# Kernel optimization log

Hardware: AMD Instinct MI355X
Metric: run time of the kernel (lower is better)

Reference implementation:

```python
import jax, jax.numpy as jnp
import numpy as np
import math

H = 12
DH = 64
MAX_POS = 1024

def setup_inputs() -> dict:
    key = jax.random.key(0)
    ks = jax.random.split(key, 8)
    B, L, D = 2, 1024, 768
    s = 0.02
    return {
        "hidden_states": jax.random.normal(ks[0], (B, L, D), jnp.float32),
        "attention_mask": jnp.zeros((B, 1, 1, L), jnp.float32),
        "struct_matrix": jax.random.uniform(ks[1], (5, B, 1, L, L), jnp.float32),
        "Wq": jax.random.normal(ks[2], (D, D), jnp.float32) * s,
        "bq": jnp.zeros((D,), jnp.float32),
        "Wk": jax.random.normal(ks[3], (D, D), jnp.float32) * s,
        "bk": jnp.zeros((D,), jnp.float32),
        "Wv": jax.random.normal(ks[4], (D, D), jnp.float32) * s,
        "bv": jnp.zeros((D,), jnp.float32),
        "dist_emb": jax.random.normal(ks[5], (2 * MAX_POS - 1, DH), jnp.float32) * s,
        "ssan_w": jax.random.normal(ks[6], (5, H, DH, DH), jnp.float32) * s,
        "abs_bias": jnp.zeros((5, H), jnp.float32),
    }

def reference(hidden_states, attention_mask, struct_matrix, Wq, bq, Wk, bk, Wv, bv, dist_emb, ssan_w, abs_bias):
    B, L, D = hidden_states.shape

    def heads(x):  # [B,L,D] -> [B,H,L,dh]
        return x.reshape(B, L, H, DH).transpose(0, 2, 1, 3)

    q = heads(hidden_states @ Wq + bq)
    k = heads(hidden_states @ Wk + bk)
    v = heads(hidden_states @ Wv + bv)

    scores = jnp.einsum('bhqd,bhkd->bhqk', q, k)

    # relative_key_query positional scores
    pos_ids = jnp.arange(L)
    distance = pos_ids[:, None] - pos_ids[None, :]          # [L,L]
    pos = dist_emb[distance + MAX_POS - 1]                  # [L,L,dh]
    scores = scores + jnp.einsum('bhld,lrd->bhlr', q, pos)
    scores = scores + jnp.einsum('bhrd,lrd->bhlr', k, pos)

    scores = scores / math.sqrt(DH)
    scores = scores + attention_mask

    # 5 SSAN bilinear bias terms, masked by structural matrices
    for i in range(5):
        bias = jnp.einsum('bhqd,hde,bhke->bhqk', q, ssan_w[i], k)
        scores = scores + (bias + abs_bias[i][None, :, None, None]) * struct_matrix[i]

    probs = jax.nn.softmax(scores, axis=-1)
    ctx = jnp.einsum('bhqk,bhkd->bqhd', probs, v).reshape(B, L, D)
    return ctx
```

## Files before the change

### kernel.cpp

```cpp
#include <hip/hip_runtime.h>
#include <math.h>

#define NB 2
#define NL 1024
#define ND 768
#define NH 12
#define DH 64

typedef _Float16 f16;
typedef _Float16 f16x4 __attribute__((ext_vector_type(4)));
typedef _Float16 f16x8 __attribute__((ext_vector_type(8)));
typedef float f32x4 __attribute__((ext_vector_type(4)));

#define MFMA16(a, b, c) __builtin_amdgcn_mfma_f32_16x16x32_f16((a), (b), (c), 0, 0, 0)

__device__ __forceinline__ void soft_barrier() {
    asm volatile("s_waitcnt lgkmcnt(0)\n\ts_barrier" ::: "memory");
}

__global__ __launch_bounds__(256) void prep_kernel(
    const float* __restrict__ hs,
    const float* __restrict__ Wq, const float* __restrict__ Wk,
    const float* __restrict__ Wv, const float* __restrict__ sw,
    const float* __restrict__ de,
    f16* __restrict__ hsf, f16* __restrict__ wt, f16* __restrict__ swt,
    f16* __restrict__ de16)
{
    __shared__ float sT[64 * 66];
    const int t = threadIdx.x;
    const int tile = blockIdx.x;

    if (tile < 768) {
        const int base = tile * 2048 + t * 8;
        float4 a = *(const float4*)&hs[base];
        float4 b = *(const float4*)&hs[base + 4];
        f16x8 hv;
        hv[0] = (f16)a.x; hv[1] = (f16)a.y; hv[2] = (f16)a.z; hv[3] = (f16)a.w;
        hv[4] = (f16)b.x; hv[5] = (f16)b.y; hv[6] = (f16)b.z; hv[7] = (f16)b.w;
        *(f16x8*)&hsf[base] = hv;
        return;
    }
    if (tile >= 1260) {
        const int base = (tile - 1260) * 2048 + t * 8;
        if (base < 2047 * 64) {
            float4 a = *(const float4*)&de[base];
            float4 b = *(const float4*)&de[base + 4];
            f16x8 hv;
            hv[0] = (f16)a.x; hv[1] = (f16)a.y; hv[2] = (f16)a.z; hv[3] = (f16)a.w;
            hv[4] = (f16)b.x; hv[5] = (f16)b.y; hv[6] = (f16)b.z; hv[7] = (f16)b.w;
            *(f16x8*)&de16[base] = hv;
        }
        return;
    }

    const float* S; f16* D; int sRS, dRS;
    const int ti = tile - 768;
    if (ti < 432) {
        const int mat = ti / 144, r2 = ti % 144, ht = r2 / 12, kt = r2 % 12;
        const float* W = (mat == 0) ? Wq : (mat == 1) ? Wk : Wv;
        S = W + (size_t)(kt * 64) * ND + ht * 64;
        D = wt + (size_t)((mat * NH + ht) * 64) * ND + kt * 64;
        sRS = ND; dRS = ND;
    } else {
        const int i = ti - 432;
        S = sw + (size_t)i * 4096;
        D = swt + (size_t)i * 4096;
        sRS = 64; dRS = 64;
    }

    {
        const int kk = t >> 2, nb = (t & 3) * 16;
        float v[16];
        #pragma unroll
        for (int j = 0; j < 4; ++j)
            *(float4*)&v[4 * j] = *(const float4*)&S[(size_t)kk * sRS + nb + 4 * j];
        #pragma unroll
        for (int jj = 0; jj < 16; ++jj)
            sT[(nb + jj) * 66 + kk] = v[jj];
    }
    soft_barrier();
    {
        const int n = t >> 2, kb = (t & 3) * 16;
        f16 tmp[16];
        #pragma unroll
        for (int j = 0; j < 8; ++j) {
            float2 x = *(float2*)&sT[n * 66 + kb + 2 * j];
            tmp[2 * j]     = (f16)x.x;
            tmp[2 * j + 1] = (f16)x.y;
        }
        *(f16x8*)&D[(size_t)n * dRS + kb]     = *(f16x8*)&tmp[0];
        *(f16x8*)&D[(size_t)n * dRS + kb + 8] = *(f16x8*)&tmp[8];
    }
}

__global__ __launch_bounds__(256, 4) void qkv_kernel(
    const f16* __restrict__ hsf, const f16* __restrict__ wt,
    const float* __restrict__ bq, const float* __restrict__ bk,
    const float* __restrict__ bv,
    f16* __restrict__ qf, f16* __restrict__ kf, f16* __restrict__ vt)
{
    __shared__ f16 sA[64 * 72], sB[64 * 72];
    __shared__ float sT[64 * 66];

    const int m0  = blockIdx.x * 64;
    const int y   = blockIdx.y;
    const int mat = y / NH, h = y % NH;
    const int t = threadIdx.x, lane = t & 63, w = t >> 6;
    const int quad = lane >> 4, l15 = lane & 15;
    const int wm = w >> 1, wn = w & 1;

    const float* bias = (mat == 0) ? bq : (mat == 1) ? bk : bv;

    f32x4 acc[2][2];
    #pragma unroll
    for (int r = 0; r < 2; ++r)
        #pragma unroll
        for (int c = 0; c < 2; ++c) acc[r][c] = (f32x4){0.f, 0.f, 0.f, 0.f};

    const int srow = t >> 2, scol = (t & 3) * 16;
    const f16* Ag = hsf + (size_t)(m0 + srow) * ND + scol;
    const f16* Bg = wt + ((size_t)y * 64 + srow) * ND + scol;

    for (int k0 = 0; k0 < ND; k0 += 64) {
        soft_barrier();
        *(f16x8*)&sA[srow * 72 + scol]     = *(const f16x8*)&Ag[k0];
        *(f16x8*)&sA[srow * 72 + scol + 8] = *(const f16x8*)&Ag[k0 + 8];
        *(f16x8*)&sB[srow * 72 + scol]     = *(const f16x8*)&Bg[k0];
        *(f16x8*)&sB[srow * 72 + scol + 8] = *(const f16x8*)&Bg[k0 + 8];
        soft_barrier();
        #pragma unroll
        for (int kk = 0; kk < 64; kk += 32) {
            const int ko = kk + quad * 8;
            f16x8 a0 = *(f16x8*)&sA[(32 * wm + l15) * 72 + ko];
            f16x8 a1 = *(f16x8*)&sA[(32 * wm + 16 + l15) * 72 + ko];
            f16x8 b0 = *(f16x8*)&sB[(32 * wn + l15) * 72 + ko];
            f16x8 b1 = *(f16x8*)&sB[(32 * wn + 16 + l15) * 72 + ko];
            acc[0][0] = MFMA16(a0, b0, acc[0][0]);
            acc[0][1] = MFMA16(a0, b1, acc[0][1]);
            acc[1][0] = MFMA16(a1, b0, acc[1][0]);
            acc[1][1] = MFMA16(a1, b1, acc[1][1]);
        }
    }
    soft_barrier();

    const int bb = m0 >> 10;
    const int lbase = m0 & 1023;
    const int bh = bb * NH + h;

    if (mat < 2) {
        #pragma unroll
        for (int r = 0; r < 2; ++r)
            #pragma unroll
            for (int c = 0; c < 2; ++c) {
                const int col = 32 * wn + 16 * c + l15;
                const float bz = bias[h * 64 + col];
                #pragma unroll
                for (int rr = 0; rr < 4; ++rr)
                    sT[(32 * wm + 16 * r + 4 * quad + rr) * 66 + col] = acc[r][c][rr] + bz;
            }
        soft_barrier();
        const int orow = t >> 2, ocb = (t & 3) * 16;
        f16 tmp[16];
        #pragma unroll
        for (int j = 0; j < 8; ++j) {
            float2 x = *(float2*)&sT[orow * 66 + ocb + 2 * j];
            tmp[2 * j] = (f16)x.x; tmp[2 * j + 1] = (f16)x.y;
        }
        f16* dst = ((mat == 0) ? qf : kf) + ((size_t)bh * NL + lbase + orow) * DH + ocb;
        *(f16x8*)dst       = *(f16x8*)&tmp[0];
        *(f16x8*)(dst + 8) = *(f16x8*)&tmp[8];
    } else {
        #pragma unroll
        for (int r = 0; r < 2; ++r)
            #pragma unroll
            for (int c = 0; c < 2; ++c) {
                const int col = 32 * wn + 16 * c + l15;
                const float bz = bias[h * 64 + col];
                #pragma unroll
                for (int rr = 0; rr < 4; ++rr)
                    sT[col * 66 + 32 * wm + 16 * r + 4 * quad + rr] = acc[r][c][rr] + bz;
            }
        soft_barrier();
        const int d = t >> 2, lcb = (t & 3) * 16;
        f16 tmp[16];
        #pragma unroll
        for (int j = 0; j < 8; ++j) {
            float2 x = *(float2*)&sT[d * 66 + lcb + 2 * j];
            tmp[2 * j] = (f16)x.x; tmp[2 * j + 1] = (f16)x.y;
        }
        f16* dst = vt + ((size_t)bh * DH + d) * NL + lbase + lcb;
        *(f16x8*)dst       = *(f16x8*)&tmp[0];
        *(f16x8*)(dst + 8) = *(f16x8*)&tmp[8];
    }
}

__global__ __launch_bounds__(256, 4) void qw_kernel(
    const f16* __restrict__ qf, const f16* __restrict__ swt,
    f16* __restrict__ qwf)
{
    __shared__ f16 sA[64 * 72], sB[64 * 72];
    __shared__ float sT[64 * 66];

    const int l0 = blockIdx.x * 64;
    const int z  = blockIdx.y;
    const int p  = z / 24, bh = z % 24, h = bh % NH;
    const int t = threadIdx.x, lane = t & 63, w = t >> 6;
    const int quad = lane >> 4, l15 = lane & 15;
    const int wm = w >> 1, wn = w & 1;

    const int srow = t >> 2, scol = (t & 3) * 16;
    {
        const f16* As = qf + ((size_t)bh * NL + l0 + srow) * DH + scol;
        const f16* Bs = swt + ((size_t)(p * NH + h) * 64 + srow) * 64 + scol;
        *(f16x8*)&sA[srow * 72 + scol]     = *(const f16x8*)As;
        *(f16x8*)&sA[srow * 72 + scol + 8] = *(const f16x8*)(As + 8);
        *(f16x8*)&sB[srow * 72 + scol]     = *(const f16x8*)Bs;
        *(f16x8*)&sB[srow * 72 + scol + 8] = *(const f16x8*)(Bs + 8);
    }
    soft_barrier();

    f32x4 acc[2][2];
    #pragma unroll
    for (int r = 0; r < 2; ++r)
        #pragma unroll
        for (int c = 0; c < 2; ++c) acc[r][c] = (f32x4){0.f, 0.f, 0.f, 0.f};

    #pragma unroll
    for (int kk = 0; kk < 64; kk += 32) {
        const int ko = kk + quad * 8;
        f16x8 a0 = *(f16x8*)&sA[(32 * wm + l15) * 72 + ko];
        f16x8 a1 = *(f16x8*)&sA[(32 * wm + 16 + l15) * 72 + ko];
        f16x8 b0 = *(f16x8*)&sB[(32 * wn + l15) * 72 + ko];
        f16x8 b1 = *(f16x8*)&sB[(32 * wn + 16 + l15) * 72 + ko];
        acc[0][0] = MFMA16(a0, b0, acc[0][0]);
        acc[0][1] = MFMA16(a0, b1, acc[0][1]);
        acc[1][0] = MFMA16(a1, b0, acc[1][0]);
        acc[1][1] = MFMA16(a1, b1, acc[1][1]);
    }
    soft_barrier();

    #pragma unroll
    for (int r = 0; r < 2; ++r)
        #pragma unroll
        for (int c = 0; c < 2; ++c) {
            const int col = 32 * wn + 16 * c + l15;
            #pragma unroll
            for (int rr = 0; rr < 4; ++rr)
                sT[(32 * wm + 16 * r + 4 * quad + rr) * 66 + col] = acc[r][c][rr];
        }
    soft_barrier();

    const int orow = t >> 2, ocb = (t & 3) * 16;
    f16 tmp[16];
    #pragma unroll
    for (int j = 0; j < 8; ++j) {
        float2 x = *(float2*)&sT[orow * 66 + ocb + 2 * j];
        tmp[2 * j] = (f16)x.x; tmp[2 * j + 1] = (f16)x.y;
    }
    f16* dst = qwf + ((size_t)(p * 24 + bh) * NL + l0 + orow) * DH + ocb;
    *(f16x8*)dst       = *(f16x8*)&tmp[0];
    *(f16x8*)(dst + 8) = *(f16x8*)&tmp[8];
}

__global__ __launch_bounds__(256, 2) void pos_kernel(
    const f16* __restrict__ qf, const f16* __restrict__ kf,
    const f16* __restrict__ de16, f16* __restrict__ posb)
{
    __shared__ f16 sQ[64 * 72], sK2[64 * 72];
    __shared__ f16 sE[128 * 72];
    __shared__ f16 sQE[64 * 140], sKE[64 * 140];

    const int l0 = blockIdx.x * 64;
    const int r0 = blockIdx.y * 64;
    const int bh = blockIdx.z;
    const int t  = threadIdx.x;
    const int lane = t & 63;
    const int w    = t >> 6;
    const int quad = lane >> 4;
    const int l15  = lane & 15;

    {
        const int row = t >> 3, col = (t & 7) * 8;
        const f16* qs = qf + ((size_t)bh * NL + l0) * DH;
        const f16* ks = kf + ((size_t)bh * NL + r0) * DH;
        *(f16x8*)&sQ[row * 72 + col]        = *(const f16x8*)&qs[row * 64 + col];
        *(f16x8*)&sQ[(row + 32) * 72 + col] = *(const f16x8*)&qs[(row + 32) * 64 + col];
        *(f16x8*)&sK2[row * 72 + col]        = *(const f16x8*)&ks[row * 64 + col];
        *(f16x8*)&sK2[(row + 32) * 72 + col] = *(const f16x8*)&ks[(row + 32) * 64 + col];
        const int ebase = l0 - r0 + 960;
        #pragma unroll
        for (int p = 0; p < 4; ++p) {
            const int er = row + 32 * p;
            if (er < 127)
                *(f16x8*)&sE[er * 72 + col] =
                    *(const f16x8*)&de16[(size_t)(ebase + er) * DH + col];
        }
    }
    soft_barrier();

    {
        const int arow = (16 * w + l15) * 72 + quad * 8;
        f16x8 aq0 = *(f16x8*)&sQ[arow];
        f16x8 aq1 = *(f16x8*)&sQ[arow + 32];
        f16x8 ak0 = *(f16x8*)&sK2[arow];
        f16x8 ak1 = *(f16x8*)&sK2[arow + 32];
        #pragma unroll
        for (int n = 0; n < 8; ++n) {
            const int brow = (16 * n + l15) * 72 + quad * 8;
            f16x8 e0 = *(f16x8*)&sE[brow];
            f16x8 e1 = *(f16x8*)&sE[brow + 32];
            f32x4 cq = {0.f, 0.f, 0.f, 0.f};
            cq = MFMA16(aq0, e0, cq);
            cq = MFMA16(aq1, e1, cq);
            f32x4 ck = {0.f, 0.f, 0.f, 0.f};
            ck = MFMA16(ak0, e0, ck);
            ck = MFMA16(ak1, e1, ck);
            #pragma unroll
            for (int r = 0; r < 4; ++r) {
                sQE[(16 * w + 4 * quad + r) * 140 + 16 * n + l15] = (f16)cq[r];
                sKE[(16 * w + 4 * quad + r) * 140 + 16 * n + l15] = (f16)ck[r];
            }
        }
    }
    soft_barrier();

    {
        const int i  = t >> 2;
        const int j0 = (t & 3) * 16;
        f16 res[16];
        #pragma unroll
        for (int jj = 0; jj < 16; ++jj) {
            const int j = j0 + jj;
            const int tt = i - j + 63;
            float v = (float)sQE[i * 140 + tt] + (float)sKE[j * 140 + tt];
            res[jj] = (f16)v;
        }
        f16* dst = posb + ((size_t)bh * NL + l0 + i) * NL + r0 + j0;
        *(f16x8*)dst       = *(f16x8*)&res[0];
        *(f16x8*)(dst + 8) = *(f16x8*)&res[8];
    }
}

__global__ __launch_bounds__(256, 2) void attn_kernel(
    const f16* __restrict__ qf, const f16* __restrict__ kf,
    const f16* __restrict__ vt, const f16* __restrict__ qwf,
    const float* __restrict__ mask, const float* __restrict__ struct_m,
    const f16* __restrict__ posb, const float* __restrict__ abs_bias,
    float* __restrict__ out)
{
    __shared__ f16 sK[64 * 72];
    __shared__ f16 sVt[2][64 * 72];
    __shared__ float sS[32 * 68];
    __shared__ f16 sP[32 * 72];
    __shared__ float sAlpha[32], sL[32];

    const int l0 = blockIdx.x * 32;
    const int bh = blockIdx.y;
    const int bb = bh / NH, h = bh % NH;
    const int t  = threadIdx.x;
    const int lane  = t & 63;
    const int w     = t >> 6;
    const int quad  = lane >> 4;
    const int l15   = lane & 15;
    const int msub  = w >> 1;
    const int npair = w & 1;

    const size_t NQKV = (size_t)NB * NH * NL * DH;

    f16x8 aQ[2], aW[5][2];
    {
        const size_t qrow = ((size_t)bh * NL + l0 + 16 * msub + l15) * DH;
        #pragma unroll
        for (int K = 0; K < 2; ++K) {
            aQ[K] = *(const f16x8*)&qf[qrow + 32 * K + 8 * quad];
            #pragma unroll
            for (int p = 0; p < 5; ++p)
                aW[p][K] = *(const f16x8*)&qwf[p * NQKV + qrow + 32 * K + 8 * quad];
        }
    }

    float ab[5];
    #pragma unroll
    for (int p = 0; p < 5; ++p) ab[p] = abs_bias[p * NH + h];

    float pf_st[5][2][4], pf_pos[2][4], pf_mask[2];

    auto stage_kv = [&](int r0s, int buf) {
        const int row = t >> 3, col = (t & 7) * 8;
        const f16* ks = kf + ((size_t)bh * NL + r0s) * DH;
        *(f16x8*)&sK[row * 72 + col]        = *(const f16x8*)&ks[row * 64 + col];
        *(f16x8*)&sK[(row + 32) * 72 + col] = *(const f16x8*)&ks[(row + 32) * 64 + col];
        const f16* vs = vt + (size_t)bh * DH * NL + r0s;
        *(f16x8*)&sVt[buf][row * 72 + col] =
            *(const f16x8*)&vs[(size_t)row * NL + col];
        *(f16x8*)&sVt[buf][(row + 32) * 72 + col] =
            *(const f16x8*)&vs[(size_t)(row + 32) * NL + col];
    };

    auto prefetch = [&](int r0s) {
        #pragma unroll
        for (int n = 0; n < 2; ++n) {
            const int j = 32 * npair + 16 * n + l15;
            pf_mask[n] = mask[bb * NL + r0s + j];
            #pragma unroll
            for (int r = 0; r < 4; ++r) {
                const int i = 16 * msub + 4 * quad + r;
                pf_pos[n][r] = (float)posb[((size_t)bh * NL + l0 + i) * NL + r0s + j];
                #pragma unroll
                for (int p = 0; p < 5; ++p)
                    pf_st[p][n][r] =
                        struct_m[((size_t)(p * NB + bb) * NL + l0 + i) * NL + r0s + j];
            }
        }
    };

    stage_kv(0, 0);
    prefetch(0);

    const int sm_i = t >> 3;
    const int sm_jb = t & 7;
    float m_cur = -INFINITY, l_cur = 0.f;
    f32x4 O[2];
    O[0] = (f32x4){0.f, 0.f, 0.f, 0.f};
    O[1] = (f32x4){0.f, 0.f, 0.f, 0.f};

    for (int kt = 0; kt < 16; ++kt) {
        const int cur = kt & 1;
        soft_barrier();

        {
            f32x4 acc[2][6];
            #pragma unroll
            for (int n = 0; n < 2; ++n)
                #pragma unroll
                for (int p = 0; p < 6; ++p)
                    acc[n][p] = (f32x4){0.f, 0.f, 0.f, 0.f};

            #pragma unroll
            for (int K = 0; K < 2; ++K) {
                const int koff = K * 32 + quad * 8;
                f16x8 bk2[2];
                #pragma unroll
                for (int n = 0; n < 2; ++n)
                    bk2[n] = *(f16x8*)&sK[(32 * npair + 16 * n + l15) * 72 + koff];
                #pragma unroll
                for (int n = 0; n < 2; ++n)
                    acc[n][0] = MFMA16(aQ[K], bk2[n], acc[n][0]);
                #pragma unroll
                for (int p = 0; p < 5; ++p)
                    #pragma unroll
                    for (int n = 0; n < 2; ++n)
                        acc[n][1 + p] = MFMA16(aW[p][K], bk2[n], acc[n][1 + p]);
            }

            #pragma unroll
            for (int n = 0; n < 2; ++n) {
                const int j = 32 * npair + 16 * n + l15;
                #pragma unroll
                for (int r = 0; r < 4; ++r) {
                    const int i = 16 * msub + 4 * quad + r;
                    float s = (acc[n][0][r] + pf_pos[n][r]) * 0.125f + pf_mask[n];
                    #pragma unroll
                    for (int p = 0; p < 5; ++p)
                        s += (acc[n][1 + p][r] + ab[p]) * pf_st[p][n][r];
                    sS[i * 68 + j] = s;
                }
            }
        }
        soft_barrier();

        {
            float sv[8];
            float smax = -INFINITY;
            #pragma unroll
            for (int k = 0; k < 8; ++k) {
                sv[k] = sS[sm_i * 68 + sm_jb + 8 * k];
                smax = fmaxf(smax, sv[k]);
            }
            #pragma unroll
            for (int off = 4; off > 0; off >>= 1)
                smax = fmaxf(smax, __shfl_xor(smax, off, 8));
            const float m_new = fmaxf(m_cur, smax);
            const float alpha = __expf(m_cur - m_new);
            float rsum = 0.f;
            #pragma unroll
            for (int k = 0; k < 8; ++k) {
                float p = __expf(sv[k] - m_new);
                sP[sm_i * 72 + sm_jb + 8 * k] = (f16)p;
                rsum += p;
            }
            #pragma unroll
            for (int off = 4; off > 0; off >>= 1)
                rsum += __shfl_xor(rsum, off, 8);
            l_cur = l_cur * alpha + rsum;
            m_cur = m_new;
            if (sm_jb == 0) { sAlpha[sm_i] = alpha; sL[sm_i] = l_cur; }
        }
        soft_barrier();

        {
            if (kt < 15) {
                stage_kv((kt + 1) * 64, cur ^ 1);
                prefetch((kt + 1) * 64);
            }

            float a4[4];
            #pragma unroll
            for (int r = 0; r < 4; ++r) a4[r] = sAlpha[16 * msub + 4 * quad + r];
            #pragma unroll
            for (int n = 0; n < 2; ++n)
                #pragma unroll
                for (int r = 0; r < 4; ++r) O[n][r] *= a4[r];

            const int prow = (16 * msub + l15) * 72;
            #pragma unroll
            for (int K = 0; K < 2; ++K) {
                const int koff = K * 32 + quad * 8;
                f16x8 pfr = *(f16x8*)&sP[prow + koff];
                #pragma unroll
                for (int n = 0; n < 2; ++n) {
                    f16x8 vfr = *(f16x8*)&sVt[cur][(32 * npair + 16 * n + l15) * 72 + koff];
                    O[n] = MFMA16(pfr, vfr, O[n]);
                }
            }
        }
    }

    float linv[4];
    #pragma unroll
    for (int r = 0; r < 4; ++r) linv[r] = 1.0f / sL[16 * msub + 4 * quad + r];
    #pragma unroll
    for (int n = 0; n < 2; ++n) {
        const int dh = 32 * npair + 16 * n + l15;
        #pragma unroll
        for (int r = 0; r < 4; ++r) {
            const int i = 16 * msub + 4 * quad + r;
            out[((size_t)bb * NL + l0 + i) * ND + h * DH + dh] = O[n][r] * linv[r];
        }
    }
}

extern "C" void kernel_launch(void* const* d_in, const int* in_sizes, int n_in,
                              void* d_out, int out_size, void* d_ws, size_t ws_size,
                              hipStream_t stream) {
    const float* hs   = (const float*)d_in[0];
    const float* mask = (const float*)d_in[1];
    const float* stm  = (const float*)d_in[2];
    const float* Wq   = (const float*)d_in[3];
    const float* bq   = (const float*)d_in[4];
    const float* Wk   = (const float*)d_in[5];
    const float* bk   = (const float*)d_in[6];
    const float* Wv   = (const float*)d_in[7];
    const float* bv   = (const float*)d_in[8];
    const float* de   = (const float*)d_in[9];
    const float* sw   = (const float*)d_in[10];
    const float* abb  = (const float*)d_in[11];
    float* outp = (float*)d_out;

    const size_t NQKV = (size_t)NB * NH * NL * DH;
    char* ws = (char*)d_ws;
    f16* qf   = (f16*)ws;                 ws += NQKV * 2;
    f16* kf   = (f16*)ws;                 ws += NQKV * 2;
    f16* vtb  = (f16*)ws;                 ws += NQKV * 2;
    f16* qwf  = (f16*)ws;                 ws += 5 * NQKV * 2;
    f16* posb = (f16*)ws;                 ws += (size_t)24 * 1024 * 1024 * 2;
    f16* de16 = (f16*)ws;
    f16* hsf = posb;
    f16* wt  = hsf + NQKV;
    f16* swt = wt + (size_t)2304 * 768;

    prep_kernel<<<1324, 256, 0, stream>>>(hs, Wq, Wk, Wv, sw, de,
                                          hsf, wt, swt, de16);
    qkv_kernel<<<dim3(32, 36), 256, 0, stream>>>(hsf, wt, bq, bk, bv, qf, kf, vtb);
    qw_kernel<<<dim3(16, 120), 256, 0, stream>>>(qf, swt, qwf);
    pos_kernel<<<dim3(16, 16, 24), 256, 0, stream>>>(qf, kf, de16, posb);
    attn_kernel<<<dim3(32, 24), 256, 0, stream>>>(qf, kf, vtb, qwf,
                                                  mask, stm, posb, abb, outp);
}
```

Baseline: 246.0 us.

## Fuse relative-position score computation into attention kernel, drop posb buffer

Removes the separate pos_kernel, which wrote a 24x1024x1024 fp16 positional-score matrix, and computes the q·E and k·E relative-position products inside the attention kernel for each 32x64 tile. Each tile stages the 95 needed distance-embedding rows into shared memory and runs extra MFMAs, then gathers along the diagonal. This avoids a large global write and read round trip. In exchange it adds MFMA work, an extra barrier per tile, and more shared memory, which could lower occupancy.

New measurement: 243.2 us. No clear change (-1.2%).

```diff
diff --git a/kernel.cpp b/kernel.cpp
--- a/kernel.cpp
+++ b/kernel.cpp
@@ -262,94 +262,18 @@
     *(f16x8*)(dst + 8) = *(f16x8*)&tmp[8];
 }
 
-__global__ __launch_bounds__(256, 2) void pos_kernel(
-    const f16* __restrict__ qf, const f16* __restrict__ kf,
-    const f16* __restrict__ de16, f16* __restrict__ posb)
-{
-    __shared__ f16 sQ[64 * 72], sK2[64 * 72];
-    __shared__ f16 sE[128 * 72];
-    __shared__ f16 sQE[64 * 140], sKE[64 * 140];
-
-    const int l0 = blockIdx.x * 64;
-    const int r0 = blockIdx.y * 64;
-    const int bh = blockIdx.z;
-    const int t  = threadIdx.x;
-    const int lane = t & 63;
-    const int w    = t >> 6;
-    const int quad = lane >> 4;
-    const int l15  = lane & 15;
-
-    {
-        const int row = t >> 3, col = (t & 7) * 8;
-        const f16* qs = qf + ((size_t)bh * NL + l0) * DH;
-        const f16* ks = kf + ((size_t)bh * NL + r0) * DH;
-        *(f16x8*)&sQ[row * 72 + col]        = *(const f16x8*)&qs[row * 64 + col];
-        *(f16x8*)&sQ[(row + 32) * 72 + col] = *(const f16x8*)&qs[(row + 32) * 64 + col];
-        *(f16x8*)&sK2[row * 72 + col]        = *(const f16x8*)&ks[row * 64 + col];
-        *(f16x8*)&sK2[(row + 32) * 72 + col] = *(const f16x8*)&ks[(row + 32) * 64 + col];
-        const int ebase = l0 - r0 + 960;
-        #pragma unroll
-        for (int p = 0; p < 4; ++p) {
-            const int er = row + 32 * p;
-            if (er < 127)
-                *(f16x8*)&sE[er * 72 + col] =
-                    *(const f16x8*)&de16[(size_t)(ebase + er) * DH + col];
-        }
-    }
-    soft_barrier();
-
-    {
-        const int arow = (16 * w + l15) * 72 + quad * 8;
-        f16x8 aq0 = *(f16x8*)&sQ[arow];
-        f16x8 aq1 = *(f16x8*)&sQ[arow + 32];
-        f16x8 ak0 = *(f16x8*)&sK2[arow];
-        f16x8 ak1 = *(f16x8*)&sK2[arow + 32];
-        #pragma unroll
-        for (int n = 0; n < 8; ++n) {
-            const int brow = (16 * n + l15) * 72 + quad * 8;
-            f16x8 e0 = *(f16x8*)&sE[brow];
-            f16x8 e1 = *(f16x8*)&sE[brow + 32];
-            f32x4 cq = {0.f, 0.f, 0.f, 0.f};
-            cq = MFMA16(aq0, e0, cq);
-            cq = MFMA16(aq1, e1, cq);
-            f32x4 ck = {0.f, 0.f, 0.f, 0.f};
-            ck = MFMA16(ak0, e0, ck);
-            ck = MFMA16(ak1, e1, ck);
-            #pragma unroll
-            for (int r = 0; r < 4; ++r) {
-                sQE[(16 * w + 4 * quad + r) * 140 + 16 * n + l15] = (f16)cq[r];
-                sKE[(16 * w + 4 * quad + r) * 140 + 16 * n + l15] = (f16)ck[r];
-            }
-        }
-    }
-    soft_barrier();
-
-    {
-        const int i  = t >> 2;
-        const int j0 = (t & 3) * 16;
-        f16 res[16];
-        #pragma unroll
-        for (int jj = 0; jj < 16; ++jj) {
-            const int j = j0 + jj;
-            const int tt = i - j + 63;
-            float v = (float)sQE[i * 140 + tt] + (float)sKE[j * 140 + tt];
-            res[jj] = (f16)v;
-        }
-        f16* dst = posb + ((size_t)bh * NL + l0 + i) * NL + r0 + j0;
-        *(f16x8*)dst       = *(f16x8*)&res[0];
-        *(f16x8*)(dst + 8) = *(f16x8*)&res[8];
-    }
-}
-
 __global__ __launch_bounds__(256, 2) void attn_kernel(
     const f16* __restrict__ qf, const f16* __restrict__ kf,
     const f16* __restrict__ vt, const f16* __restrict__ qwf,
     const float* __restrict__ mask, const float* __restrict__ struct_m,
-    const f16* __restrict__ posb, const float* __restrict__ abs_bias,
+    const f16* __restrict__ de16, const float* __restrict__ abs_bias,
     float* __restrict__ out)
 {
     __shared__ f16 sK[64 * 72];
     __shared__ f16 sVt[2][64 * 72];
+    __shared__ f16 sE[96 * 72];
+    __shared__ f16 sQEl[96 * 34];
+    __shared__ f16 sKEl[96 * 66];
     __shared__ float sS[32 * 68];
     __shared__ f16 sP[32 * 72];
     __shared__ float sAlpha[32], sL[32];
@@ -383,7 +307,7 @@
     #pragma unroll
     for (int p = 0; p < 5; ++p) ab[p] = abs_bias[p * NH + h];
 
-    float pf_st[5][2][4], pf_pos[2][4], pf_mask[2];
+    float pf_st[5][2][4], pf_mask[2];
 
     auto stage_kv = [&](int r0s, int buf) {
         const int row = t >> 3, col = (t & 7) * 8;
@@ -397,6 +321,18 @@
             *(const f16x8*)&vs[(size_t)(row + 32) * NL + col];
     };
 
+    auto stage_E = [&](int r0s) {
+        const int ebase = l0 - r0s + 960;
+        #pragma unroll
+        for (int p = 0; p < 3; ++p) {
+            const int idx = t + 256 * p;
+            const int er = idx >> 3, col = (idx & 7) * 8;
+            if (er < 95)
+                *(f16x8*)&sE[er * 72 + col] =
+                    *(const f16x8*)&de16[(size_t)(ebase + er) * DH + col];
+        }
+    };
+
     auto prefetch = [&](int r0s) {
         #pragma unroll
         for (int n = 0; n < 2; ++n) {
@@ -405,7 +341,6 @@
             #pragma unroll
             for (int r = 0; r < 4; ++r) {
                 const int i = 16 * msub + 4 * quad + r;
-                pf_pos[n][r] = (float)posb[((size_t)bh * NL + l0 + i) * NL + r0s + j];
                 #pragma unroll
                 for (int p = 0; p < 5; ++p)
                     pf_st[p][n][r] =
@@ -415,6 +350,7 @@
     };
 
     stage_kv(0, 0);
+    stage_E(0);
     prefetch(0);
 
     const int sm_i = t >> 3;
@@ -429,6 +365,35 @@
         soft_barrier();
 
         {
+            f16x8 ak0 = *(f16x8*)&sK[(16 * w + l15) * 72 + quad * 8];
+            f16x8 ak1 = *(f16x8*)&sK[(16 * w + l15) * 72 + 32 + quad * 8];
+            #pragma unroll
+            for (int c = 0; c < 3; ++c) {
+                const int nt = 3 * npair + c;
+                f16x8 e0 = *(f16x8*)&sE[(16 * nt + l15) * 72 + quad * 8];
+                f16x8 e1 = *(f16x8*)&sE[(16 * nt + l15) * 72 + 32 + quad * 8];
+                f32x4 cq = {0.f, 0.f, 0.f, 0.f};
+                cq = MFMA16(aQ[0], e0, cq);
+                cq = MFMA16(aQ[1], e1, cq);
+                #pragma unroll
+                for (int r = 0; r < 4; ++r)
+                    sQEl[(16 * nt + l15) * 34 + 16 * msub + 4 * quad + r] = (f16)cq[r];
+            }
+            #pragma unroll
+            for (int nt = 0; nt < 6; ++nt) {
+                f16x8 e0 = *(f16x8*)&sE[(16 * nt + l15) * 72 + quad * 8];
+                f16x8 e1 = *(f16x8*)&sE[(16 * nt + l15) * 72 + 32 + quad * 8];
+                f32x4 ck = {0.f, 0.f, 0.f, 0.f};
+                ck = MFMA16(ak0, e0, ck);
+                ck = MFMA16(ak1, e1, ck);
+                #pragma unroll
+                for (int r = 0; r < 4; ++r)
+                    sKEl[(16 * nt + l15) * 66 + 16 * w + 4 * quad + r] = (f16)ck[r];
+            }
+        }
+        soft_barrier();
+
+        {
             f32x4 acc[2][6];
             #pragma unroll
             for (int n = 0; n < 2; ++n)
@@ -459,7 +424,9 @@
                 #pragma unroll
                 for (int r = 0; r < 4; ++r) {
                     const int i = 16 * msub + 4 * quad + r;
-                    float s = (acc[n][0][r] + pf_pos[n][r]) * 0.125f + pf_mask[n];
+                    const int tp = i - j + 63;
+                    float posv = (float)sQEl[tp * 34 + i] + (float)sKEl[tp * 66 + j];
+                    float s = (acc[n][0][r] + posv) * 0.125f + pf_mask[n];
                     #pragma unroll
                     for (int p = 0; p < 5; ++p)
                         s += (acc[n][1 + p][r] + ab[p]) * pf_st[p][n][r];
@@ -501,6 +468,7 @@
         {
             if (kt < 15) {
                 stage_kv((kt + 1) * 64, cur ^ 1);
+                stage_E((kt + 1) * 64);
                 prefetch((kt + 1) * 64);
             }
 
@@ -563,17 +531,15 @@
     f16* kf   = (f16*)ws;                 ws += NQKV * 2;
     f16* vtb  = (f16*)ws;                 ws += NQKV * 2;
     f16* qwf  = (f16*)ws;                 ws += 5 * NQKV * 2;
-    f16* posb = (f16*)ws;                 ws += (size_t)24 * 1024 * 1024 * 2;
+    f16* hsf  = (f16*)ws;                 ws += NQKV * 2;
+    f16* wt   = (f16*)ws;                 ws += (size_t)2304 * 768 * 2;
+    f16* swt  = (f16*)ws;                 ws += (size_t)245760 * 2;
     f16* de16 = (f16*)ws;
-    f16* hsf = posb;
-    f16* wt  = hsf + NQKV;
-    f16* swt = wt + (size_t)2304 * 768;
 
     prep_kernel<<<1324, 256, 0, stream>>>(hs, Wq, Wk, Wv, sw, de,
                                           hsf, wt, swt, de16);
     qkv_kernel<<<dim3(32, 36), 256, 0, stream>>>(hsf, wt, bq, bk, bv, qf, kf, vtb);
     qw_kernel<<<dim3(16, 120), 256, 0, stream>>>(qf, swt, qwf);
-    pos_kernel<<<dim3(16, 16, 24), 256, 0, stream>>>(qf, kf, de16, posb);
     attn_kernel<<<dim3(32, 24), 256, 0, stream>>>(qf, kf, vtb, qwf,
-                                                  mask, stm, posb, abb, outp);
+                                                  mask, stm, de16, abb, outp);
 }
```
